# Kernel tuning notes

Measured on AMD Instinct MI355X. Metric: run time of the kernel, lower is better.

The kernel has to match this reference:

```python
import jax, jax.numpy as jnp
import numpy as np

N, N2, N3 = 40000, 20000, 10000
E, E2, E3 = 640000, 320000, 160000
HEADS = 4
F_IN = 5


def _glorot(k, shape):
    lim = float(np.sqrt(6.0 / (shape[0] + shape[-1])))
    return jax.random.uniform(k, shape, jnp.float32, -lim, lim)


def setup_inputs() -> dict:
    key = jax.random.key(0)
    ks = jax.random.split(key, 40)
    inp = {}
    inp["x"] = jax.random.normal(ks[0], (N, F_IN), jnp.float32)
    inp["edge_index"] = jax.random.randint(ks[1], (2, E), 0, N)
    inp["edge_index2"] = jax.random.randint(ks[2], (2, E2), 0, N2)
    inp["edge_index3"] = jax.random.randint(ks[3], (2, E3), 0, N3)
    # graclus-style cluster maps; constructed surjective so no cluster is empty
    inp["cluster1"] = jax.random.permutation(ks[4], jnp.arange(N) % N2)
    inp["cluster2"] = jax.random.permutation(ks[5], jnp.arange(N2) % N3)
    dims = [(F_IN, 16), (16, 32), (32, 64), (64, 32), (64, 16)]
    i = 6
    for idx, (fi, fo) in enumerate(dims, 1):
        inp[f"cW{idx}"] = _glorot(ks[i], (fi, HEADS * fo)); i += 1
        inp[f"cU{idx}"] = _glorot(ks[i], (fi, HEADS)); i += 1
        inp[f"cc{idx}"] = jnp.zeros((HEADS,), jnp.float32)
        inp[f"cb{idx}"] = jnp.zeros((fo,), jnp.float32)
    inp["l1W"] = _glorot(ks[i], (32, 256)); i += 1
    inp["l1b"] = jnp.zeros((256,), jnp.float32)
    inp["l2W"] = _glorot(ks[i], (256, 6890)); i += 1
    inp["l2b"] = jnp.zeros((6890,), jnp.float32)
    inp["oW"] = _glorot(ks[i], (6890, 1)); i += 1
    inp["ob"] = jnp.zeros((1,), jnp.float32)
    return inp


def feast_conv(x, ei, W, U, c, b, n, fo):
    """PyG FeaStConv: self-loops, per-edge head-softmax attention, mean aggregation."""
    sl = jnp.arange(n)
    src = jnp.concatenate([ei[0], sl])  # message sources (x_j)
    dst = jnp.concatenate([ei[1], sl])  # aggregation targets (x_i)
    xs, xd = x[src], x[dst]
    q = jax.nn.softmax((xs - xd) @ U + c, axis=-1)          # [E+n, H]
    m = (xs @ W).reshape(-1, HEADS, fo)                      # [E+n, H, fo]
    msg = jnp.einsum('eh,eho->eo', q, m)                     # [E+n, fo]
    agg = jax.ops.segment_sum(msg, dst, num_segments=n)
    cnt = jax.ops.segment_sum(jnp.ones((dst.shape[0],), x.dtype), dst, num_segments=n)
    return agg / cnt[:, None] + b


def _forward(x, edge_index, edge_index2, edge_index3, cluster1, cluster2, p):
    x1 = jax.nn.relu(feast_conv(x, edge_index, p["cW1"], p["cU1"], p["cc1"], p["cb1"], N, 16))
    x2 = jax.ops.segment_max(x1, cluster1, num_segments=N2)                     # graclus max_pool
    x2 = jax.nn.relu(feast_conv(x2, edge_index2, p["cW2"], p["cU2"], p["cc2"], p["cb2"], N2, 32))
    x3 = jax.ops.segment_max(x2, cluster2, num_segments=N3)
    x3 = jax.nn.relu(feast_conv(x3, edge_index3, p["cW3"], p["cU3"], p["cc3"], p["cb3"], N3, 64))
    x3 = jax.nn.relu(feast_conv(x3, edge_index3, p["cW4"], p["cU4"], p["cc4"], p["cb4"], N3, 32))
    x3 = jnp.concatenate([x2, x3[cluster2]], axis=1)                            # [N2, 64] unpool+skip
    x3 = jax.nn.relu(feast_conv(x3, edge_index2, p["cW5"], p["cU5"], p["cc5"], p["cb5"], N2, 16))
    h = jnp.concatenate([x1, x3[cluster1]], axis=1)                             # [N, 32]
    h = jax.nn.relu(h @ p["l1W"] + p["l1b"])
    h = jax.nn.relu(h @ p["l2W"] + p["l2b"])                                   # [N, 6890]
    return jax.nn.sigmoid(h @ p["oW"] + p["ob"])                                # [N, 1]


def reference(x, edge_index, edge_index2, edge_index3, cluster1, cluster2,
              cW1, cU1, cc1, cb1, cW2, cU2, cc2, cb2, cW3, cU3, cc3, cb3,
              cW4, cU4, cc4, cb4, cW5, cU5, cc5, cb5, l1W, l1b, l2W, l2b, oW, ob):
    p = dict(cW1=cW1, cU1=cU1, cc1=cc1, cb1=cb1, cW2=cW2, cU2=cU2, cc2=cc2, cb2=cb2,
             cW3=cW3, cU3=cU3, cc3=cc3, cb3=cb3, cW4=cW4, cU4=cU4, cc4=cc4, cb4=cb4,
             cW5=cW5, cU5=cU5, cc5=cc5, cb5=cb5, l1W=l1W, l1b=l1b, l2W=l2W, l2b=l2b,
             oW=oW, ob=ob)
    return _forward(x, edge_index, edge_index2, edge_index3, cluster1, cluster2, p)
```

## Files before the change

kernel.cpp:

```cpp
#include <hip/hip_runtime.h>
#include <math.h>

#define N1  40000
#define NN2 20000
#define NN3 10000
#define EE1 640000
#define EE2 320000
#define EE3 160000
#define ET  (EE1 + EE2 + EE3)
#define JPAD 6912
#define JREAL 6890
#define NTILE 432
#define CSPLIT 8
#define TPB (NTILE/CSPLIT)
#define NSTG (TPB/2)
#define NROWP 40192
#define NGRP 628
#define CAP 64
#define PBK 864

typedef __attribute__((ext_vector_type(8))) short short8;
typedef __attribute__((ext_vector_type(4))) float f32x4;
typedef unsigned short u16;

__device__ inline unsigned short f2bf(float f) {
  unsigned u = __float_as_uint(f);
  u += 0x7FFF + ((u >> 16) & 1);
  return (unsigned short)(u >> 16);
}

__device__ inline f32x4 qsoft(f32x4 xs, f32x4 xd, float c0, float c1, float c2, float c3) {
  float l0 = xs[0] - xd[0] + c0, l1 = xs[1] - xd[1] + c1;
  float l2 = xs[2] - xd[2] + c2, l3 = xs[3] - xd[3] + c3;
  float mx = fmaxf(fmaxf(l0, l1), fmaxf(l2, l3));
  float q0 = __expf(l0 - mx), q1 = __expf(l1 - mx);
  float q2 = __expf(l2 - mx), q3 = __expf(l3 - mx);
  float iv = 1.f / (q0 + q1 + q2 + q3);
  return (f32x4){q0 * iv, q1 * iv, q2 * iv, q3 * iv};
}

__global__ void k_matmulWU(const float* __restrict__ Xa, int fa,
                           const float* __restrict__ Xb, int fb,
                           const int* __restrict__ map,
                           const float* __restrict__ W, const float* __restrict__ U,
                           float* __restrict__ xW, float* __restrict__ xU,
                           int n, int co) {
  int ct = co + 4;
  int idx = blockIdx.x * 256 + threadIdx.x;
  if (idx >= n * ct) return;
  int row = idx / ct, col = idx - row * ct;
  const float* M;
  int stride;
  if (col < co) { M = W + col; stride = co; }
  else          { M = U + (col - co); stride = 4; }
  float s = 0.f;
  const float* ar = Xa + (size_t)row * fa;
  for (int k = 0; k < fa; ++k) s = fmaf(ar[k], M[(size_t)k * stride], s);
  if (Xb) {
    const float* br = Xb + (size_t)map[row] * fb;
    for (int k = 0; k < fb; ++k) s = fmaf(br[k], M[(size_t)(fa + k) * stride], s);
  }
  if (col < co) xW[(size_t)row * co + col] = s;
  else          xU[(size_t)row * 4 + (col - co)] = s;
}

__global__ void k_xU(const float* __restrict__ xin, const float* __restrict__ U,
                     float* __restrict__ xu, int n, int ci) {
  int idx = blockIdx.x * 256 + threadIdx.x;
  if (idx >= n * 4) return;
  int h = idx & 3, d = idx >> 2;
  const float* xr = xin + (size_t)d * ci;
  float s = 0.f;
  for (int k = 0; k < ci; ++k) s = fmaf(xr[k], U[k * 4 + h], s);
  xu[idx] = s;
}

__global__ __launch_bounds__(256) void k_setup(
    const float* __restrict__ l2W, short8* __restrict__ Bp,
    const float* __restrict__ l2b, const float* __restrict__ oW,
    float* __restrict__ l2bp, float* __restrict__ oWp,
    const int* __restrict__ ei1, const int* __restrict__ ei2,
    const int* __restrict__ ei3,
    int* __restrict__ c1, int* __restrict__ c2, int* __restrict__ c3,
    u16* __restrict__ s1, u16* __restrict__ s2, u16* __restrict__ s3,
    const float* __restrict__ x, float* __restrict__ x8,
    const float* __restrict__ U1, float* __restrict__ xu1) {
  __shared__ float tile[32][65];
  const int bid = blockIdx.x, tid = threadIdx.x;
  if (bid < PBK) {
    if (bid < 27) {
      int j = bid * 256 + tid;
      l2bp[j] = (j < JREAL) ? l2b[j] : 0.f;
      oWp[j]  = (j < JREAL) ? oW[j]  : 0.f;
    }
    const int kg = bid / 108, jg = bid - kg * 108;
    const int k0 = kg * 32, j0 = jg * 64;
    const int kr = tid >> 6, jc = tid & 63;
    const int j = j0 + jc;
#pragma unroll
    for (int i = 0; i < 8; ++i) {
      int row = kr * 8 + i;
      tile[row][jc] = (j < JREAL) ? l2W[(size_t)(k0 + row) * JREAL + j] : 0.f;
    }
    __syncthreads();
    const int tt = tid >> 6, lane = tid & 63;
    short8 v;
#pragma unroll
    for (int i = 0; i < 8; ++i)
      v[i] = (short)f2bf(tile[((lane >> 4) << 3) + i][tt * 16 + (lane & 15)]);
    Bp[((size_t)(jg * 4 + tt) * 8 + kg) * 64 + lane] = v;
    return;
  }
  int i = (bid - PBK) * 256 + tid;
  if (i < ET) {
    int e = i;
    const int* ei; int* cnt; u16* sl; int E;
    if (e < EE1) { ei = ei1; cnt = c1; sl = s1; E = EE1; }
    else {
      e -= EE1;
      if (e < EE2) { ei = ei2; cnt = c2; sl = s2; E = EE2; }
      else { e -= EE2; ei = ei3; cnt = c3; sl = s3; E = EE3; }
    }
    int s = ei[e], d = ei[E + e];
    int pos = atomicAdd(&cnt[d], 1);
    if (pos < CAP) sl[(size_t)d * CAP + pos] = (u16)s;
    return;
  }
  i -= ET;
  if (i < N1 * 8) {
    int d = i >> 3, k = i & 7;
    x8[i] = (k < 5) ? x[d * 5 + k] : 0.f;
    return;
  }
  i -= N1 * 8;
  if (i < N1 * 4) {
    int h = i & 3, d = i >> 2;
    const float* xr = x + (size_t)d * 5;
    float s = 0.f;
#pragma unroll
    for (int k = 0; k < 5; ++k) s = fmaf(xr[k], U1[k * 4 + h], s);
    xu1[i] = s;
  }
}

template<int CI4, int FO, int KREAL, bool XUOUT>
__global__ __launch_bounds__(256) void k_aggf(
    const int* __restrict__ cnt, const u16* __restrict__ slots,
    const float* __restrict__ xU, const f32x4* __restrict__ xin4, int stride4,
    const float* __restrict__ c, const float* __restrict__ W,
    const float* __restrict__ b, float* __restrict__ outp, int n,
    const int* __restrict__ pool_cl, int* __restrict__ pool_out,
    const float* __restrict__ Unext, float* __restrict__ xunext) {
  constexpr int LPN = CI4 * 4;
  constexpr int NB  = 256 / LPN;
  __shared__ float sh[NB][CI4 * 16];
  __shared__ float sh2[NB][FO];
  const int tid = threadIdx.x;
  const int nl = tid / LPN, li = tid - nl * LPN;
  const int cg = li >> 2, sp = li & 3;
  const int d = blockIdx.x * NB + nl;
  const float c0 = c[0], c1 = c[1], c2 = c[2], c3 = c[3];
  const f32x4* XU4 = (const f32x4*)xU;

  if (d < n) {
    const f32x4 xd = XU4[d];
    const int deg = min(cnt[d], CAP);
    const int jlo = (deg * sp) >> 2, jhi = (deg * (sp + 1)) >> 2;
    const u16* sl = slots + (size_t)d * CAP;
    f32x4 acc[4];
#pragma unroll
    for (int e = 0; e < 4; ++e) acc[e] = (f32x4){0.f, 0.f, 0.f, 0.f};
    int j = jlo;
    for (; j + 4 <= jhi; j += 4) {
      int s0 = sl[j], s1 = sl[j + 1], s2 = sl[j + 2], s3 = sl[j + 3];
      f32x4 u0 = XU4[s0], u1 = XU4[s1], u2 = XU4[s2], u3 = XU4[s3];
      f32x4 v0 = xin4[(size_t)s0 * stride4 + cg];
      f32x4 v1 = xin4[(size_t)s1 * stride4 + cg];
      f32x4 v2 = xin4[(size_t)s2 * stride4 + cg];
      f32x4 v3 = xin4[(size_t)s3 * stride4 + cg];
      f32x4 q0 = qsoft(u0, xd, c0, c1, c2, c3);
      f32x4 q1 = qsoft(u1, xd, c0, c1, c2, c3);
      f32x4 q2 = qsoft(u2, xd, c0, c1, c2, c3);
      f32x4 q3 = qsoft(u3, xd, c0, c1, c2, c3);
#pragma unroll
      for (int e = 0; e < 4; ++e)
        acc[e] += v0[e] * q0 + v1[e] * q1 + v2[e] * q2 + v3[e] * q3;
    }
    for (; j < jhi; ++j) {
      int s = sl[j];
      f32x4 u = XU4[s];
      f32x4 v = xin4[(size_t)s * stride4 + cg];
      f32x4 q = qsoft(u, xd, c0, c1, c2, c3);
#pragma unroll
      for (int e = 0; e < 4; ++e) acc[e] += v[e] * q;
    }
#pragma unroll
    for (int e = 0; e < 4; ++e)
#pragma unroll
      for (int h = 0; h < 4; ++h) {
        acc[e][h] += __shfl_xor(acc[e][h], 1);
        acc[e][h] += __shfl_xor(acc[e][h], 2);
      }
    if (sp == 0) {
      float mx = fmaxf(fmaxf(c0, c1), fmaxf(c2, c3));
      float q0 = __expf(c0 - mx), q1 = __expf(c1 - mx);
      float q2 = __expf(c2 - mx), q3 = __expf(c3 - mx);
      float iv = 1.f / (q0 + q1 + q2 + q3);
      f32x4 q = (f32x4){q0 * iv, q1 * iv, q2 * iv, q3 * iv};
      f32x4 xv = xin4[(size_t)d * stride4 + cg];
#pragma unroll
      for (int e = 0; e < 4; ++e) {
        f32x4 a = acc[e] + xv[e] * q;
#pragma unroll
        for (int h = 0; h < 4; ++h) sh[nl][(cg * 4 + e) * 4 + h] = a[h];
      }
    }
  }
  __syncthreads();

  constexpr int NBFO = NB * FO;
#pragma unroll
  for (int base = 0; base < NBFO; base += 256) {
    int i2 = base + tid;
    if (i2 < NBFO) {
      int ln = i2 / FO, o = i2 - ln * FO;
      int d2 = blockIdx.x * NB + ln;
      if (d2 < n) {
        float acc2 = 0.f;
        const float* shl = sh[ln];
        for (int k = 0; k < KREAL; ++k) {
          const float* wr = W + (size_t)k * (4 * FO) + o;
          acc2 += shl[k * 4 + 0] * wr[0] + shl[k * 4 + 1] * wr[FO]
                + shl[k * 4 + 2] * wr[2 * FO] + shl[k * 4 + 3] * wr[3 * FO];
        }
        int deg2 = min(cnt[d2], CAP);
        float v = fmaxf(acc2 / (float)(deg2 + 1) + b[o], 0.f);
        outp[(size_t)d2 * FO + o] = v;
        if (XUOUT) sh2[ln][o] = v;
        if (pool_cl)
          atomicMax((int*)&pool_out[(size_t)pool_cl[d2] * FO + o], __float_as_int(v));
      }
    }
  }

  if (XUOUT) {
    __syncthreads();
    if (tid < NB * 4) {
      int ln = tid >> 2, h = tid & 3;
      int d3 = blockIdx.x * NB + ln;
      if (d3 < n) {
        float s = 0.f;
        const float* so = sh2[ln];
        for (int o = 0; o < FO; ++o) s = fmaf(so[o], Unext[o * 4 + h], s);
        xunext[(size_t)d3 * 4 + h] = s;
      }
    }
  }
}

__global__ void k_attagg4(const int* __restrict__ cnt, const u16* __restrict__ slots,
                          const float* __restrict__ xU, const float4* __restrict__ xW,
                          const float* __restrict__ c, const float4* __restrict__ b4,
                          float4* __restrict__ outp, int n, int fo4,
                          const int* __restrict__ pool_cl, int* __restrict__ pool_out) {
  int idx = blockIdx.x * 256 + threadIdx.x;
  if (idx >= n * fo4 * 4) return;
  const int sp = idx & 3;
  const int t = idx >> 2;
  const int d = t / fo4, og = t - d * fo4;
  const float c0 = c[0], c1 = c[1], c2 = c[2], c3 = c[3];
  const f32x4* XU4 = (const f32x4*)xU;
  const f32x4 xd = XU4[d];
  const int deg = min(cnt[d], CAP);
  const int jlo = (deg * sp) >> 2;
  const int jhi = (deg * (sp + 1)) >> 2;
  const u16* sl = slots + (size_t)d * CAP;
  f32x4 acc = (f32x4){0.f, 0.f, 0.f, 0.f};
  float ax = 0.f, ay = 0.f, az = 0.f, aw = 0.f;
  int j = jlo;
  for (; j + 4 <= jhi; j += 4) {
    int s0 = sl[j], s1 = sl[j + 1], s2 = sl[j + 2], s3 = sl[j + 3];
    f32x4 u0 = XU4[s0], u1 = XU4[s1], u2 = XU4[s2], u3 = XU4[s3];
    const float4* m0p = xW + (size_t)s0 * 4 * fo4 + og;
    const float4* m1p = xW + (size_t)s1 * 4 * fo4 + og;
    const float4* m2p = xW + (size_t)s2 * 4 * fo4 + og;
    const float4* m3p = xW + (size_t)s3 * 4 * fo4 + og;
    float4 a0 = m0p[0], a1 = m0p[fo4], a2 = m0p[2 * fo4], a3 = m0p[3 * fo4];
    float4 b0 = m1p[0], b1 = m1p[fo4], b2 = m1p[2 * fo4], b3 = m1p[3 * fo4];
    float4 g0 = m2p[0], g1 = m2p[fo4], g2 = m2p[2 * fo4], g3 = m2p[3 * fo4];
    float4 h0 = m3p[0], h1 = m3p[fo4], h2 = m3p[2 * fo4], h3 = m3p[3 * fo4];
    f32x4 q0 = qsoft(u0, xd, c0, c1, c2, c3);
    f32x4 q1 = qsoft(u1, xd, c0, c1, c2, c3);
    f32x4 q2 = qsoft(u2, xd, c0, c1, c2, c3);
    f32x4 q3 = qsoft(u3, xd, c0, c1, c2, c3);
    ax += q0[0]*a0.x + q0[1]*a1.x + q0[2]*a2.x + q0[3]*a3.x
        + q1[0]*b0.x + q1[1]*b1.x + q1[2]*b2.x + q1[3]*b3.x
        + q2[0]*g0.x + q2[1]*g1.x + q2[2]*g2.x + q2[3]*g3.x
        + q3[0]*h0.x + q3[1]*h1.x + q3[2]*h2.x + q3[3]*h3.x;
    ay += q0[0]*a0.y + q0[1]*a1.y + q0[2]*a2.y + q0[3]*a3.y
        + q1[0]*b0.y + q1[1]*b1.y + q1[2]*b2.y + q1[3]*b3.y
        + q2[0]*g0.y + q2[1]*g1.y + q2[2]*g2.y + q2[3]*g3.y
        + q3[0]*h0.y + q3[1]*h1.y + q3[2]*h2.y + q3[3]*h3.y;
    az += q0[0]*a0.z + q0[1]*a1.z + q0[2]*a2.z + q0[3]*a3.z
        + q1[0]*b0.z + q1[1]*b1.z + q1[2]*b2.z + q1[3]*b3.z
        + q2[0]*g0.z + q2[1]*g1.z + q2[2]*g2.z + q2[3]*g3.z
        + q3[0]*h0.z + q3[1]*h1.z + q3[2]*h2.z + q3[3]*h3.z;
    aw += q0[0]*a0.w + q0[1]*a1.w + q0[2]*a2.w + q0[3]*a3.w
        + q1[0]*b0.w + q1[1]*b1.w + q1[2]*b2.w + q1[3]*b3.w
        + q2[0]*g0.w + q2[1]*g1.w + q2[2]*g2.w + q2[3]*g3.w
        + q3[0]*h0.w + q3[1]*h1.w + q3[2]*h2.w + q3[3]*h3.w;
  }
  for (; j < jhi; ++j) {
    int s = sl[j];
    f32x4 u = XU4[s];
    const float4* m = xW + (size_t)s * 4 * fo4 + og;
    float4 m0 = m[0], m1 = m[fo4], m2 = m[2 * fo4], m3 = m[3 * fo4];
    f32x4 q = qsoft(u, xd, c0, c1, c2, c3);
    ax += q[0] * m0.x + q[1] * m1.x + q[2] * m2.x + q[3] * m3.x;
    ay += q[0] * m0.y + q[1] * m1.y + q[2] * m2.y + q[3] * m3.y;
    az += q[0] * m0.z + q[1] * m1.z + q[2] * m2.z + q[3] * m3.z;
    aw += q[0] * m0.w + q[1] * m1.w + q[2] * m2.w + q[3] * m3.w;
  }
  ax += __shfl_xor(ax, 1); ay += __shfl_xor(ay, 1);
  az += __shfl_xor(az, 1); aw += __shfl_xor(aw, 1);
  ax += __shfl_xor(ax, 2); ay += __shfl_xor(ay, 2);
  az += __shfl_xor(az, 2); aw += __shfl_xor(aw, 2);
  if (sp) return;
  {
    float mx = fmaxf(fmaxf(c0, c1), fmaxf(c2, c3));
    float q0 = __expf(c0 - mx), q1 = __expf(c1 - mx);
    float q2 = __expf(c2 - mx), q3 = __expf(c3 - mx);
    float inv = 1.f / (q0 + q1 + q2 + q3);
    const float4* m = xW + (size_t)d * 4 * fo4 + og;
    float4 m0 = m[0], m1 = m[fo4], m2 = m[2 * fo4], m3 = m[3 * fo4];
    ax += (q0 * m0.x + q1 * m1.x + q2 * m2.x + q3 * m3.x) * inv;
    ay += (q0 * m0.y + q1 * m1.y + q2 * m2.y + q3 * m3.y) * inv;
    az += (q0 * m0.z + q1 * m1.z + q2 * m2.z + q3 * m3.z) * inv;
    aw += (q0 * m0.w + q1 * m1.w + q2 * m2.w + q3 * m3.w) * inv;
  }
  const float inv = 1.f / (float)(deg + 1);
  const float4 bb = b4[og];
  float4 v;
  v.x = fmaxf(ax * inv + bb.x, 0.f);
  v.y = fmaxf(ay * inv + bb.y, 0.f);
  v.z = fmaxf(az * inv + bb.z, 0.f);
  v.w = fmaxf(aw * inv + bb.w, 0.f);
  outp[(size_t)d * fo4 + og] = v;
  if (pool_cl) {
    int* po = pool_out + ((size_t)pool_cl[d] * fo4 + og) * 4;
    atomicMax(&po[0], __float_as_int(v.x));
    atomicMax(&po[1], __float_as_int(v.y));
    atomicMax(&po[2], __float_as_int(v.z));
    atomicMax(&po[3], __float_as_int(v.w));
  }
}

__global__ __launch_bounds__(256) void k_packh(
    const float* __restrict__ x1, const float* __restrict__ x5,
    const int* __restrict__ cl1, const float* __restrict__ l1W,
    const float* __restrict__ l1b, short8* __restrict__ Apack) {
  __shared__ float h1s[64][256];
  const int tid = threadIdx.x;
  const int row0 = blockIdx.x * 64;

  float wcol[32];
#pragma unroll
  for (int k = 0; k < 32; ++k) wcol[k] = l1W[k * 256 + tid];
  const float bt = l1b[tid];

  for (int r = 0; r < 64; ++r) {
    const int row = row0 + r;
    float s = bt;
    if (row < N1) {
      const float* a = x1 + (size_t)row * 16;
      const float* b = x5 + (size_t)cl1[row] * 16;
#pragma unroll
      for (int k = 0; k < 16; ++k) s = fmaf(a[k], wcol[k], s);
#pragma unroll
      for (int k = 0; k < 16; ++k) s = fmaf(b[k], wcol[16 + k], s);
    }
    h1s[r][tid ^ ((r & 7) << 3)] = fmaxf(s, 0.f);
  }
  __syncthreads();

#pragma unroll
  for (int j = 0; j < 8; ++j) {
    int s = j * 256 + tid;
    int l = s & 63, ks = (s >> 6) & 7, rb = s >> 9;
    int row = rb * 16 + (l & 15);
    int col0 = (ks * 32 + ((l >> 4) << 3)) ^ ((row & 7) << 3);
    const float* sp = &h1s[row][col0];
    short8 v;
#pragma unroll
    for (int i = 0; i < 8; ++i) v[i] = (short)f2bf(sp[i]);
    Apack[(size_t)blockIdx.x * 2048 + s] = v;
  }
}

__global__ __launch_bounds__(256, 2) void k_final2(
    const short8* __restrict__ Apack, const short8* __restrict__ Bp,
    const float* __restrict__ l2bp, const float* __restrict__ oWp,
    float* __restrict__ zbuf) {
  __shared__ short8 bufs[2][1024];
  const int tid = threadIdx.x, wid = tid >> 6, l = tid & 63;
  const int rg = blockIdx.x >> 3, cg = blockIdx.x & 7;
  const int lm = l & 15, lh = l >> 4;

  short8 af[4][8];
  {
    const short8* ap = Apack + (size_t)(rg * 4 + wid) * 2048 + l;
#pragma unroll
    for (int rb = 0; rb < 4; ++rb)
#pragma unroll
      for (int ks = 0; ks < 8; ++ks) af[rb][ks] = ap[rb * 512 + ks * 64];
  }

  const short8* bsrc = Bp + (size_t)cg * TPB * 512;
  short8 n0 = bsrc[tid], n1 = bsrc[256 + tid], n2 = bsrc[512 + tid], n3 = bsrc[768 + tid];
  bufs[0][tid] = n0; bufs[0][256 + tid] = n1;
  bufs[0][512 + tid] = n2; bufs[0][768 + tid] = n3;
  {
    const short8* p = bsrc + 1024;
    n0 = p[tid]; n1 = p[256 + tid]; n2 = p[512 + tid]; n3 = p[768 + tid];
  }
  asm volatile("s_waitcnt lgkmcnt(0)" ::: "memory");
  __builtin_amdgcn_s_barrier();
  asm volatile("" ::: "memory");

  float zp[4][4];
#pragma unroll
  for (int rb = 0; rb < 4; ++rb)
#pragma unroll
    for (int r = 0; r < 4; ++r) zp[rb][r] = 0.f;

  for (int st = 0; st < NSTG; ++st) {
    const int cur = st & 1;
    if (st + 1 < NSTG) {
      bufs[cur ^ 1][tid] = n0; bufs[cur ^ 1][256 + tid] = n1;
      bufs[cur ^ 1][512 + tid] = n2; bufs[cur ^ 1][768 + tid] = n3;
    }
    if (st + 2 < NSTG) {
      const short8* p = bsrc + (st + 2) * 1024;
      n0 = p[tid]; n1 = p[256 + tid]; n2 = p[512 + tid]; n3 = p[768 + tid];
    }
#pragma unroll
    for (int half = 0; half < 2; ++half) {
      short8 bfr[8];
#pragma unroll
      for (int ks = 0; ks < 8; ++ks) bfr[ks] = bufs[cur][half * 512 + ks * 64 + l];

      f32x4 acc[4];
#pragma unroll
      for (int rb = 0; rb < 4; ++rb) acc[rb] = (f32x4){0.f, 0.f, 0.f, 0.f};
      __builtin_amdgcn_s_setprio(1);
#pragma unroll
      for (int ks = 0; ks < 8; ++ks)
#pragma unroll
        for (int rb = 0; rb < 4; ++rb)
          acc[rb] = __builtin_amdgcn_mfma_f32_16x16x32_bf16(af[rb][ks], bfr[ks], acc[rb], 0, 0, 0);
      __builtin_amdgcn_s_setprio(0);

      const int j = (cg * TPB + st * 2 + half) * 16 + lm;
      const float lb = l2bp[j];
      const float ow = oWp[j];
#pragma unroll
      for (int rb = 0; rb < 4; ++rb)
#pragma unroll
        for (int r = 0; r < 4; ++r)
          zp[rb][r] += fmaxf(acc[rb][r] + lb, 0.f) * ow;
    }
    asm volatile("s_waitcnt lgkmcnt(0)" ::: "memory");
    __builtin_amdgcn_s_barrier();
    asm volatile("" ::: "memory");
  }

#pragma unroll
  for (int m = 1; m < 16; m <<= 1)
#pragma unroll
    for (int rb = 0; rb < 4; ++rb)
#pragma unroll
      for (int r = 0; r < 4; ++r)
        zp[rb][r] += __shfl_xor(zp[rb][r], m);

  if (lm == 0) {
    const int rbase = rg * 256 + wid * 64 + lh * 4;
#pragma unroll
    for (int rb = 0; rb < 4; ++rb)
#pragma unroll
      for (int r = 0; r < 4; ++r)
        atomicAdd(&zbuf[rbase + rb * 16 + r], zp[rb][r]);
  }
}

__global__ void k_sigm(const float* __restrict__ zbuf, const float* __restrict__ ob,
                       float* __restrict__ out) {
  int i = blockIdx.x * 256 + threadIdx.x;
  if (i >= N1) return;
  out[i] = 1.f / (1.f + expf(-(zbuf[i] + ob[0])));
}

extern "C" void kernel_launch(void* const* d_in, const int* in_sizes, int n_in,
                              void* d_out, int out_size, void* d_ws, size_t ws_size,
                              hipStream_t stream) {
  const float* x   = (const float*)d_in[0];
  const int* ei1   = (const int*)d_in[1];
  const int* ei2   = (const int*)d_in[2];
  const int* ei3   = (const int*)d_in[3];
  const int* cl1   = (const int*)d_in[4];
  const int* cl2   = (const int*)d_in[5];
  const float* cW1 = (const float*)d_in[6],  *cU1 = (const float*)d_in[7],
             * cc1 = (const float*)d_in[8],  *cb1 = (const float*)d_in[9];
  const float* cW2 = (const float*)d_in[10], *cU2 = (const float*)d_in[11],
             * cc2 = (const float*)d_in[12], *cb2 = (const float*)d_in[13];
  const float* cW3 = (const float*)d_in[14], *cU3 = (const float*)d_in[15],
             * cc3 = (const float*)d_in[16], *cb3 = (const float*)d_in[17];
  const float* cW4 = (const float*)d_in[18], *cU4 = (const float*)d_in[19],
             * cc4 = (const float*)d_in[20], *cb4 = (const float*)d_in[21];
  const float* cW5 = (const float*)d_in[22], *cU5 = (const float*)d_in[23],
             * cc5 = (const float*)d_in[24], *cb5 = (const float*)d_in[25];
  const float* l1W = (const float*)d_in[26], *l1b = (const float*)d_in[27];
  const float* l2W = (const float*)d_in[28], *l2b = (const float*)d_in[29];
  const float* oW  = (const float*)d_in[30], *ob  = (const float*)d_in[31];

  float* ws = (float*)d_ws;
  float* x2p  = ws + 0;
  float* x3p  = ws + 320000;
  float* zbuf = ws + 640000;
  int*  cnt1  = (int*)(ws + 680192);
  int*  cnt2  = (int*)(ws + 720192);
  int*  cnt3  = (int*)(ws + 740192);
  float* x1   = ws + 750192;
  float* x2   = ws + 1390192;
  float* x5   = ws + 2030192;
  short8* Bp  = (short8*)(ws + 2350192);
  float* l2bp = ws + 3234928;
  float* oWp  = ws + 3241840;
  u16*  sl1   = (u16*)(ws + 3248752);
  u16*  sl2   = (u16*)(ws + 4528752);
  u16*  sl3   = (u16*)(ws + 5168752);
  float* x3a  = ws + 5488752;
  float* x3b  = ws + 6128752;
  float* x8   = ws + 6448752;
  float* xu   = ws + 6768752;
  float* xub  = ws + 6928752;
  float* xW   = ws + 6968752;
  short8* Apack = (short8*)(ws + 3248752);

  hipMemsetAsync(ws, 0, 750192 * sizeof(float), stream);

  const int prepThreads = ET + N1 * 8 + N1 * 4;
  k_setup<<<PBK + (prepThreads + 255) / 256, 256, 0, stream>>>(
      l2W, Bp, l2b, oW, l2bp, oWp,
      ei1, ei2, ei3, cnt1, cnt2, cnt3, sl1, sl2, sl3, x, x8, cU1, xu);

  k_aggf<2, 16, 5, false><<<(N1 + 31) / 32, 256, 0, stream>>>(
      cnt1, sl1, xu, (const f32x4*)x8, 2, cc1, cW1, cb1, x1, N1, cl1, (int*)x2p,
      nullptr, nullptr);
  k_xU<<<(NN2 * 4 + 255) / 256, 256, 0, stream>>>(x2p, cU2, xu, NN2, 16);
  k_aggf<4, 32, 16, false><<<(NN2 + 15) / 16, 256, 0, stream>>>(
      cnt2, sl2, xu, (const f32x4*)x2p, 4, cc2, cW2, cb2, x2, NN2, cl2, (int*)x3p,
      nullptr, nullptr);
  k_xU<<<(NN3 * 4 + 255) / 256, 256, 0, stream>>>(x3p, cU3, xu, NN3, 32);
  k_aggf<8, 64, 32, true><<<(NN3 + 7) / 8, 256, 0, stream>>>(
      cnt3, sl3, xu, (const f32x4*)x3p, 8, cc3, cW3, cb3, x3a, NN3, nullptr, nullptr,
      cU4, xub);
  k_aggf<16, 32, 64, false><<<(NN3 + 3) / 4, 256, 0, stream>>>(
      cnt3, sl3, xub, (const f32x4*)x3a, 16, cc4, cW4, cb4, x3b, NN3, nullptr, nullptr,
      nullptr, nullptr);
  k_matmulWU<<<(NN2 * 68 + 255) / 256, 256, 0, stream>>>(x2, 32, x3b, 32, cl2,
                                                         cW5, cU5, xW, xu, NN2, 64);
  k_attagg4<<<(NN2 * 4 * 4 + 255) / 256, 256, 0, stream>>>(
      cnt2, sl2, xu, (const float4*)xW, cc5, (const float4*)cb5, (float4*)x5, NN2, 4,
      nullptr, nullptr);

  k_packh<<<NGRP, 256, 0, stream>>>(x1, x5, cl1, l1W, l1b, Apack);
  k_final2<<<(NROWP / 256) * CSPLIT, 256, 0, stream>>>(Apack, Bp, l2bp, oWp, zbuf);
  k_sigm<<<(N1 + 255) / 256, 256, 0, stream>>>(zbuf, ob, (float*)d_out);
}
```

Baseline: 411.8 us.

## Interleave attention logits with node features in one combined row buffer

Stores each node's 4-head U-projection next to its features in one padded row (xU first, then features), so each gathered neighbour's logits and features come from the same cache lines instead of two separate arrays. Setup, pooling atomics, the xU kernels and the conv kernels now read and write this combined layout through new stride and offset parameters. This cuts scattered gather traffic in the aggregation kernels. The cost is wider rows, a larger zeroed region, and row strides that are not powers of two.

```diff
diff --git a/kernel.cpp b/kernel.cpp
--- a/kernel.cpp
+++ b/kernel.cpp
@@ -64,15 +64,15 @@
   else          xU[(size_t)row * 4 + (col - co)] = s;
 }
 
-__global__ void k_xU(const float* __restrict__ xin, const float* __restrict__ U,
-                     float* __restrict__ xu, int n, int ci) {
+__global__ void k_xUc(float* __restrict__ xc, const float* __restrict__ U,
+                      int n, int ci, int stridef) {
   int idx = blockIdx.x * 256 + threadIdx.x;
   if (idx >= n * 4) return;
   int h = idx & 3, d = idx >> 2;
-  const float* xr = xin + (size_t)d * ci;
+  const float* xr = xc + (size_t)d * stridef + 4;
   float s = 0.f;
   for (int k = 0; k < ci; ++k) s = fmaf(xr[k], U[k * 4 + h], s);
-  xu[idx] = s;
+  xc[(size_t)d * stridef + h] = s;
 }
 
 __global__ __launch_bounds__(256) void k_setup(
@@ -83,8 +83,8 @@
     const int* __restrict__ ei3,
     int* __restrict__ c1, int* __restrict__ c2, int* __restrict__ c3,
     u16* __restrict__ s1, u16* __restrict__ s2, u16* __restrict__ s3,
-    const float* __restrict__ x, float* __restrict__ x8,
-    const float* __restrict__ U1, float* __restrict__ xu1) {
+    const float* __restrict__ x, const float* __restrict__ U1,
+    float* __restrict__ xc1) {
   __shared__ float tile[32][65];
   const int bid = blockIdx.x, tid = threadIdx.x;
   if (bid < PBK) {
@@ -127,32 +127,37 @@
     return;
   }
   i -= ET;
-  if (i < N1 * 8) {
-    int d = i >> 3, k = i & 7;
-    x8[i] = (k < 5) ? x[d * 5 + k] : 0.f;
-    return;
-  }
-  i -= N1 * 8;
-  if (i < N1 * 4) {
-    int h = i & 3, d = i >> 2;
-    const float* xr = x + (size_t)d * 5;
-    float s = 0.f;
-#pragma unroll
-    for (int k = 0; k < 5; ++k) s = fmaf(xr[k], U1[k * 4 + h], s);
-    xu1[i] = s;
+  if (i < N1 * 12) {
+    int d = i / 12, k = i - d * 12;
+    float v;
+    if (k < 4) {
+      const float* xr = x + (size_t)d * 5;
+      float s = 0.f;
+#pragma unroll
+      for (int kk = 0; kk < 5; ++kk) s = fmaf(xr[kk], U1[kk * 4 + k], s);
+      v = s;
+    } else if (k < 9) {
+      v = x[(size_t)d * 5 + (k - 4)];
+    } else {
+      v = 0.f;
+    }
+    xc1[i] = v;
   }
 }
 
 template<int CI4, int FO, int KREAL, bool XUOUT>
 __global__ __launch_bounds__(256) void k_aggf(
     const int* __restrict__ cnt, const u16* __restrict__ slots,
-    const float* __restrict__ xU, const f32x4* __restrict__ xin4, int stride4,
+    const f32x4* __restrict__ xc,
     const float* __restrict__ c, const float* __restrict__ W,
-    const float* __restrict__ b, float* __restrict__ outp, int n,
-    const int* __restrict__ pool_cl, int* __restrict__ pool_out,
-    const float* __restrict__ Unext, float* __restrict__ xunext) {
+    const float* __restrict__ b,
+    float* __restrict__ outp, int out_stride, int out_off, int n,
+    const int* __restrict__ pool_cl, float* __restrict__ pool_base,
+    int pool_stride, int pool_off,
+    const float* __restrict__ Unext, float* __restrict__ xunext, int xu_stride) {
   constexpr int LPN = CI4 * 4;
   constexpr int NB  = 256 / LPN;
+  constexpr int STRC = CI4 + 1;
   __shared__ float sh[NB][CI4 * 16];
   __shared__ float sh2[NB][FO];
   const int tid = threadIdx.x;
@@ -160,10 +165,9 @@
   const int cg = li >> 2, sp = li & 3;
   const int d = blockIdx.x * NB + nl;
   const float c0 = c[0], c1 = c[1], c2 = c[2], c3 = c[3];
-  const f32x4* XU4 = (const f32x4*)xU;
 
   if (d < n) {
-    const f32x4 xd = XU4[d];
+    const f32x4 xd = xc[(size_t)d * STRC];
     const int deg = min(cnt[d], CAP);
     const int jlo = (deg * sp) >> 2, jhi = (deg * (sp + 1)) >> 2;
     const u16* sl = slots + (size_t)d * CAP;
@@ -173,11 +177,12 @@
     int j = jlo;
     for (; j + 4 <= jhi; j += 4) {
       int s0 = sl[j], s1 = sl[j + 1], s2 = sl[j + 2], s3 = sl[j + 3];
-      f32x4 u0 = XU4[s0], u1 = XU4[s1], u2 = XU4[s2], u3 = XU4[s3];
-      f32x4 v0 = xin4[(size_t)s0 * stride4 + cg];
-      f32x4 v1 = xin4[(size_t)s1 * stride4 + cg];
-      f32x4 v2 = xin4[(size_t)s2 * stride4 + cg];
-      f32x4 v3 = xin4[(size_t)s3 * stride4 + cg];
+      f32x4 u0 = xc[(size_t)s0 * STRC], u1 = xc[(size_t)s1 * STRC];
+      f32x4 u2 = xc[(size_t)s2 * STRC], u3 = xc[(size_t)s3 * STRC];
+      f32x4 v0 = xc[(size_t)s0 * STRC + 1 + cg];
+      f32x4 v1 = xc[(size_t)s1 * STRC + 1 + cg];
+      f32x4 v2 = xc[(size_t)s2 * STRC + 1 + cg];
+      f32x4 v3 = xc[(size_t)s3 * STRC + 1 + cg];
       f32x4 q0 = qsoft(u0, xd, c0, c1, c2, c3);
       f32x4 q1 = qsoft(u1, xd, c0, c1, c2, c3);
       f32x4 q2 = qsoft(u2, xd, c0, c1, c2, c3);
@@ -188,8 +193,8 @@
     }
     for (; j < jhi; ++j) {
       int s = sl[j];
-      f32x4 u = XU4[s];
-      f32x4 v = xin4[(size_t)s * stride4 + cg];
+      f32x4 u = xc[(size_t)s * STRC];
+      f32x4 v = xc[(size_t)s * STRC + 1 + cg];
       f32x4 q = qsoft(u, xd, c0, c1, c2, c3);
 #pragma unroll
       for (int e = 0; e < 4; ++e) acc[e] += v[e] * q;
@@ -207,7 +212,7 @@
       float q2 = __expf(c2 - mx), q3 = __expf(c3 - mx);
       float iv = 1.f / (q0 + q1 + q2 + q3);
       f32x4 q = (f32x4){q0 * iv, q1 * iv, q2 * iv, q3 * iv};
-      f32x4 xv = xin4[(size_t)d * stride4 + cg];
+      f32x4 xv = xc[(size_t)d * STRC + 1 + cg];
 #pragma unroll
       for (int e = 0; e < 4; ++e) {
         f32x4 a = acc[e] + xv[e] * q;
@@ -235,10 +240,11 @@
         }
         int deg2 = min(cnt[d2], CAP);
         float v = fmaxf(acc2 / (float)(deg2 + 1) + b[o], 0.f);
-        outp[(size_t)d2 * FO + o] = v;
+        outp[(size_t)d2 * out_stride + out_off + o] = v;
         if (XUOUT) sh2[ln][o] = v;
         if (pool_cl)
-          atomicMax((int*)&pool_out[(size_t)pool_cl[d2] * FO + o], __float_as_int(v));
+          atomicMax((int*)&pool_base[(size_t)pool_cl[d2] * pool_stride + pool_off + o],
+                    __float_as_int(v));
       }
     }
   }
@@ -252,7 +258,7 @@
         float s = 0.f;
         const float* so = sh2[ln];
         for (int o = 0; o < FO; ++o) s = fmaf(so[o], Unext[o * 4 + h], s);
-        xunext[(size_t)d3 * 4 + h] = s;
+        xunext[(size_t)d3 * xu_stride + h] = s;
       }
     }
   }
@@ -275,7 +281,6 @@
   const int jlo = (deg * sp) >> 2;
   const int jhi = (deg * (sp + 1)) >> 2;
   const u16* sl = slots + (size_t)d * CAP;
-  f32x4 acc = (f32x4){0.f, 0.f, 0.f, 0.f};
   float ax = 0.f, ay = 0.f, az = 0.f, aw = 0.f;
   int j = jlo;
   for (; j + 4 <= jhi; j += 4) {
@@ -523,51 +528,49 @@
   const float* oW  = (const float*)d_in[30], *ob  = (const float*)d_in[31];
 
   float* ws = (float*)d_ws;
-  float* x2p  = ws + 0;
-  float* x3p  = ws + 320000;
-  float* zbuf = ws + 640000;
-  int*  cnt1  = (int*)(ws + 680192);
-  int*  cnt2  = (int*)(ws + 720192);
-  int*  cnt3  = (int*)(ws + 740192);
-  float* x1   = ws + 750192;
-  float* x2   = ws + 1390192;
-  float* x5   = ws + 2030192;
-  short8* Bp  = (short8*)(ws + 2350192);
-  float* l2bp = ws + 3234928;
-  float* oWp  = ws + 3241840;
-  u16*  sl1   = (u16*)(ws + 3248752);
-  u16*  sl2   = (u16*)(ws + 4528752);
-  u16*  sl3   = (u16*)(ws + 5168752);
-  float* x3a  = ws + 5488752;
-  float* x3b  = ws + 6128752;
-  float* x8   = ws + 6448752;
+  float* xc2  = ws + 0;
+  float* xc3  = ws + 400000;
+  float* zbuf = ws + 760000;
+  int*  cnt1  = (int*)(ws + 800192);
+  int*  cnt2  = (int*)(ws + 840192);
+  int*  cnt3  = (int*)(ws + 860192);
+  float* x1   = ws + 870192;
+  float* x2   = ws + 1510192;
+  float* x5   = ws + 2150192;
+  short8* Bp  = (short8*)(ws + 2470192);
+  float* l2bp = ws + 3354928;
+  float* oWp  = ws + 3361840;
+  u16*  sl1   = (u16*)(ws + 3368752);
+  u16*  sl2   = (u16*)(ws + 4648752);
+  u16*  sl3   = (u16*)(ws + 5288752);
+  float* xc1  = ws + 5608752;
+  float* xc4b = ws + 6088752;
   float* xu   = ws + 6768752;
-  float* xub  = ws + 6928752;
-  float* xW   = ws + 6968752;
-  short8* Apack = (short8*)(ws + 3248752);
-
-  hipMemsetAsync(ws, 0, 750192 * sizeof(float), stream);
-
-  const int prepThreads = ET + N1 * 8 + N1 * 4;
+  float* xW   = ws + 6848752;
+  short8* Apack = (short8*)(ws + 3368752);
+
+  hipMemsetAsync(ws, 0, 870192 * sizeof(float), stream);
+
+  const int prepThreads = ET + N1 * 12;
   k_setup<<<PBK + (prepThreads + 255) / 256, 256, 0, stream>>>(
       l2W, Bp, l2b, oW, l2bp, oWp,
-      ei1, ei2, ei3, cnt1, cnt2, cnt3, sl1, sl2, sl3, x, x8, cU1, xu);
+      ei1, ei2, ei3, cnt1, cnt2, cnt3, sl1, sl2, sl3, x, cU1, xc1);
 
   k_aggf<2, 16, 5, false><<<(N1 + 31) / 32, 256, 0, stream>>>(
-      cnt1, sl1, xu, (const f32x4*)x8, 2, cc1, cW1, cb1, x1, N1, cl1, (int*)x2p,
-      nullptr, nullptr);
-  k_xU<<<(NN2 * 4 + 255) / 256, 256, 0, stream>>>(x2p, cU2, xu, NN2, 16);
+      cnt1, sl1, (const f32x4*)xc1, cc1, cW1, cb1, x1, 16, 0, N1,
+      cl1, xc2, 20, 4, nullptr, nullptr, 0);
+  k_xUc<<<(NN2 * 4 + 255) / 256, 256, 0, stream>>>(xc2, cU2, NN2, 16, 20);
   k_aggf<4, 32, 16, false><<<(NN2 + 15) / 16, 256, 0, stream>>>(
-      cnt2, sl2, xu, (const f32x4*)x2p, 4, cc2, cW2, cb2, x2, NN2, cl2, (int*)x3p,
-      nullptr, nullptr);
-  k_xU<<<(NN3 * 4 + 255) / 256, 256, 0, stream>>>(x3p, cU3, xu, NN3, 32);
+      cnt2, sl2, (const f32x4*)xc2, cc2, cW2, cb2, x2, 32, 0, NN2,
+      cl2, xc3, 36, 4, nullptr, nullptr, 0);
+  k_xUc<<<(NN3 * 4 + 255) / 256, 256, 0, stream>>>(xc3, cU3, NN3, 32, 36);
   k_aggf<8, 64, 32, true><<<(NN3 + 7) / 8, 256, 0, stream>>>(
-      cnt3, sl3, xu, (const f32x4*)x3p, 8, cc3, cW3, cb3, x3a, NN3, nullptr, nullptr,
-      cU4, xub);
+      cnt3, sl3, (const f32x4*)xc3, cc3, cW3, cb3, xc4b, 68, 4, NN3,
+      nullptr, nullptr, 0, 0, cU4, xc4b, 68);
   k_aggf<16, 32, 64, false><<<(NN3 + 3) / 4, 256, 0, stream>>>(
-      cnt3, sl3, xub, (const f32x4*)x3a, 16, cc4, cW4, cb4, x3b, NN3, nullptr, nullptr,
-      nullptr, nullptr);
-  k_matmulWU<<<(NN2 * 68 + 255) / 256, 256, 0, stream>>>(x2, 32, x3b, 32, cl2,
+      cnt3, sl3, (const f32x4*)xc4b, cc4, cW4, cb4, xc1, 32, 0, NN3,
+      nullptr, nullptr, 0, 0, nullptr, nullptr, 0);
+  k_matmulWU<<<(NN2 * 68 + 255) / 256, 256, 0, stream>>>(x2, 32, xc1 , 32, cl2,
                                                          cW5, cU5, xW, xu, NN2, 64);
   k_attagg4<<<(NN2 * 4 * 4 + 255) / 256, 256, 0, stream>>>(
       cnt2, sl2, xu, (const float4*)xW, cc5, (const float4*)cb5, (float4*)x5, NN2, 4,
```

Measured after the change: 407.0 us, median of 2. About the same (-1.2%).
